# Optimization experiments

Hardware: AMD Instinct MI355X
Metric: run time of the kernel (lower is better)

Reference implementation:

```python
import jax, jax.numpy as jnp
import numpy as np

N_NODES = 100000
N_EDGES = 1250000
D_FEAT = 64

def setup_inputs() -> dict:
    key = jax.random.key(0)
    k1, k2, k3, k4 = jax.random.split(key, 4)
    src_x = jax.random.normal(k1, (N_NODES, D_FEAT), dtype=jnp.float32)
    dst_x = jax.random.normal(k2, (N_NODES, D_FEAT), dtype=jnp.float32)
    edge_index = jax.random.randint(k3, (2, N_EDGES), 0, N_NODES, dtype=jnp.int64)
    edge_weight = jax.random.uniform(k4, (N_EDGES, 1), dtype=jnp.float32)
    return {"src_x": src_x, "dst_x": dst_x, "edge_index": edge_index, "edge_weight": edge_weight}

def reference(src_x, dst_x, edge_index, edge_weight):
    # gather [E, d], scale by edge weight, scatter-add to destination nodes
    src_idx = edge_index[0]
    dst_idx = edge_index[1]
    msg = edge_weight * src_x[src_idx]            # [E, d]
    emb = jax.ops.segment_sum(msg, dst_idx, num_segments=dst_x.shape[0])  # [N_dst, d]
    return emb
```

## Files before the change

kernel.cpp:

```cpp
#include <hip/hip_runtime.h>

#define D_FEAT   64
#define BSHIFT   7
#define BROWS    (1 << BSHIFT)
#define SRC_MASK 0x1FFFFFF
#define CAPF     2816
#define CAPF_RAW 1920
#define OVF_CAP  16384
#define CAP_R5   2560
#define B_SC     512

__device__ __forceinline__ unsigned short f2bf(float f) {
    unsigned u = __float_as_uint(f);
    u += 0x7FFF + ((u >> 16) & 1);
    return (unsigned short)(u >> 16);
}
__device__ __forceinline__ float lo16f(unsigned u) { return __uint_as_float(u << 16); }
__device__ __forceinline__ float hi16f(unsigned u) { return __uint_as_float(u & 0xFFFF0000u); }
__device__ __forceinline__ float bf2f(unsigned short h) { return __uint_as_float(((unsigned)h) << 16); }

__global__ void lgconv_scatter_atomic(const float* __restrict__ src_x,
                                      const int* __restrict__ src_idx,
                                      const int* __restrict__ dst_idx,
                                      const float* __restrict__ ew,
                                      float* __restrict__ out,
                                      int n_edges) {
    int tid = blockIdx.x * blockDim.x + threadIdx.x;
    int edge = tid >> 4;
    int l    = tid & 15;
    if (edge >= n_edges) return;
    int s = src_idx[edge];
    int d = dst_idx[edge];
    float w = ew[edge];
    const float4 v = *reinterpret_cast<const float4*>(src_x + (size_t)s * D_FEAT + l * 4);
    float* o = out + (size_t)d * D_FEAT + l * 4;
    atomicAdd(o + 0, w * v.x);
    atomicAdd(o + 1, w * v.y);
    atomicAdd(o + 2, w * v.z);
    atomicAdd(o + 3, w * v.w);
}


__global__ void k_conv_hist(const float* __restrict__ src_x, unsigned short* __restrict__ sxb,
                            const int* __restrict__ dst, int* __restrict__ C,
                            int NE4, int E, int NB) {
    extern __shared__ int h[];
    int t = threadIdx.x, blk = blockIdx.x;
    int gsz = gridDim.x * blockDim.x;
    for (int i = blk * blockDim.x + t; i < NE4; i += gsz) {
        float4 v = reinterpret_cast<const float4*>(src_x)[i];
        ushort4 o;
        o.x = f2bf(v.x); o.y = f2bf(v.y); o.z = f2bf(v.z); o.w = f2bf(v.w);
        reinterpret_cast<ushort4*>(sxb)[i] = o;
    }
    for (int i = t; i < NB; i += blockDim.x) h[i] = 0;
    __syncthreads();
    int chunk = (E + gridDim.x - 1) / gridDim.x;
    int e0 = blk * chunk, e1 = min(E, e0 + chunk);
    for (int e = e0 + t; e < e1; e += blockDim.x)
        atomicAdd(&h[dst[e] >> BSHIFT], 1);
    __syncthreads();
    for (int i = t; i < NB; i += blockDim.x)
        C[i * B_SC + blk] = h[i];
}

__global__ void k_scan_det(int* __restrict__ C, int* __restrict__ btot,
                           int* __restrict__ ovf_cnt, int NB) {
    __shared__ int tmp[B_SC];
    int b = blockIdx.x, t = threadIdx.x;
    int v = C[b * B_SC + t];
    tmp[t] = v;
    __syncthreads();
    for (int d = 1; d < B_SC; d <<= 1) {
        int x = (t >= d) ? tmp[t - d] : 0;
        __syncthreads();
        tmp[t] += x;
        __syncthreads();
    }
    C[b * B_SC + t] = b * CAPF + tmp[t] - v;
    if (t == B_SC - 1) btot[b] = tmp[t];
    if (b == 0 && t == 0) *ovf_cnt = 0;
}

__global__ void k_scatter_det(const int* __restrict__ src, const int* __restrict__ dst,
                              const float* __restrict__ ew, const int* __restrict__ OFF,
                              int2* __restrict__ rec, int* __restrict__ ovf,
                              int* __restrict__ ovf_cnt, int E, int NB) {
    extern __shared__ int h[];
    int t = threadIdx.x, blk = blockIdx.x;
    for (int i = t; i < NB; i += blockDim.x) h[i] = OFF[i * B_SC + blk];
    __syncthreads();
    int chunk = (E + gridDim.x - 1) / gridDim.x;
    int e0 = blk * chunk, e1 = min(E, e0 + chunk);
    for (int e = e0 + t; e < e1; e += blockDim.x) {
        int d = dst[e];
        int b = d >> BSHIFT;
        int pos = atomicAdd(&h[b], 1);
        if (pos < b * CAPF + CAPF_RAW)
            rec[pos] = make_int2(src[e] | ((d & (BROWS - 1)) << 25),
                                 ((int)f2bf(ew[e])) << 16);
        else {
            int o = atomicAdd(ovf_cnt, 1);
            if (o < OVF_CAP) ovf[o] = e;
        }
    }
}

__global__ __launch_bounds__(512)
void k_sort_gather(const int* __restrict__ btot, const int2* __restrict__ rec,
                   const unsigned short* __restrict__ sxb,
                   const int* __restrict__ src, const int* __restrict__ dst,
                   const float* __restrict__ ew,
                   const int* __restrict__ ovf, const int* __restrict__ ovf_cnt,
                   float* __restrict__ out, int N) {
    __shared__ int2 S[CAPF_RAW];
    __shared__ int hist[BROWS];
    __shared__ int incl[BROWS];
    __shared__ int offl[BROWS];
    int b = blockIdx.x, t = threadIdx.x;
    int gbase = b * CAPF;
    int count = btot[b]; if (count > CAPF_RAW) count = CAPF_RAW;
    int nbase = b << BSHIFT;

    for (int i = t; i < BROWS; i += blockDim.x) hist[i] = 0;
    __syncthreads();
    for (int i = t; i < count; i += blockDim.x)
        atomicAdd(&hist[(rec[gbase + i].x >> 25) & (BROWS - 1)], 1);
    __syncthreads();
    if (t < BROWS) incl[t] = hist[t];
    __syncthreads();
    for (int d = 1; d < BROWS; d <<= 1) {
        int v = (t < BROWS && t >= d) ? incl[t - d] : 0;
        __syncthreads();
        if (t < BROWS) incl[t] += v;
        __syncthreads();
    }
    if (t < BROWS) {
        int ex = incl[t] - hist[t];
        offl[t] = ex;
        incl[t] = ex;
    }
    __syncthreads();
    for (int i = t; i < count; i += blockDim.x) {
        int2 r = rec[gbase + i];
        int pos = atomicAdd(&incl[(r.x >> 25) & (BROWS - 1)], 1);
        S[pos] = r;
    }
    __syncthreads();

    int wave = t >> 6, lane = t & 63;
    int grp = lane >> 3;
    int sub = lane & 7;

    for (int kb = wave * 16; kb < wave * 16 + 16; kb += 8) {
        int k    = kb + grp;
        int off  = offl[k];
        int deg  = hist[k];
        float a0 = 0.f, a1 = 0.f, a2 = 0.f, a3 = 0.f,
              a4 = 0.f, a5 = 0.f, a6 = 0.f, a7 = 0.f;

        for (int c = 0; __any(c < deg); c += 8) {
            int rs = 0; float rw = 0.f;
            if (c + sub < deg) {
                int2 r = S[off + c + sub];
                rs = r.x;
                rw = hi16f((unsigned)r.y);
            }
            #pragma unroll
            for (int i = 0; i < 8; ++i) {
                int jl = (grp << 3) + i;
                int   s = __shfl(rs, jl) & SRC_MASK;
                float w = __shfl(rw, jl);
                const uint4 u = *reinterpret_cast<const uint4*>(
                    sxb + (size_t)s * D_FEAT + sub * 8);
                a0 = fmaf(w, lo16f(u.x), a0); a1 = fmaf(w, hi16f(u.x), a1);
                a2 = fmaf(w, lo16f(u.y), a2); a3 = fmaf(w, hi16f(u.y), a3);
                a4 = fmaf(w, lo16f(u.z), a4); a5 = fmaf(w, hi16f(u.z), a5);
                a6 = fmaf(w, lo16f(u.w), a6); a7 = fmaf(w, hi16f(u.w), a7);
            }
        }
        int node = nbase + k;
        if (node < N) {
            float* o = out + (size_t)node * D_FEAT + sub * 8;
            *reinterpret_cast<float4*>(o)     = make_float4(a0, a1, a2, a3);
            *reinterpret_cast<float4*>(o + 4) = make_float4(a4, a5, a6, a7);
        }
    }

    __syncthreads();
    int n = *ovf_cnt; if (n > OVF_CAP) n = OVF_CAP;
    for (int idx = t; idx < n; idx += blockDim.x) {
        int e = ovf[idx];
        int d = dst[e];
        if ((d >> BSHIFT) != b) continue;
        float w = ew[e];
        int s = src[e];
        for (int q = 0; q < D_FEAT; ++q)
            atomicAdd(out + (size_t)d * D_FEAT + q,
                      w * bf2f(sxb[(size_t)s * D_FEAT + q]));
    }
}


__global__ void k_hist_b(const int* __restrict__ dst, int* __restrict__ counts_b,
                         int E, int NB) {
    extern __shared__ int h[];
    for (int i = threadIdx.x; i < NB; i += blockDim.x) h[i] = 0;
    __syncthreads();
    int chunk = (E + gridDim.x - 1) / gridDim.x;
    int e0 = blockIdx.x * chunk;
    int e1 = min(E, e0 + chunk);
    for (int e = e0 + threadIdx.x; e < e1; e += blockDim.x)
        atomicAdd(&h[dst[e] >> BSHIFT], 1);
    __syncthreads();
    for (int i = threadIdx.x; i < NB; i += blockDim.x)
        if (h[i]) atomicAdd(&counts_b[i], h[i]);
}

__global__ void k_scan_b(const int* __restrict__ counts, int* __restrict__ offsets,
                         int* __restrict__ cursor, int NB) {
    __shared__ int tmp[1024];
    __shared__ int carry;
    int t = threadIdx.x;
    if (t == 0) carry = 0;
    __syncthreads();
    for (int base = 0; base < NB; base += 1024) {
        int i = base + t;
        int v = (i < NB) ? counts[i] : 0;
        tmp[t] = v;
        __syncthreads();
        for (int d = 1; d < 1024; d <<= 1) {
            int x = (t >= d) ? tmp[t - d] : 0;
            __syncthreads();
            tmp[t] += x;
            __syncthreads();
        }
        int excl = tmp[t] - v + carry;
        if (i < NB) { offsets[i] = excl; cursor[i] = excl; }
        __syncthreads();
        if (t == 1023) carry += tmp[1023];
        __syncthreads();
    }
    if (t == 0) offsets[NB] = carry;
}

__global__ void k_scatter_b(const int* __restrict__ src, const int* __restrict__ dst,
                            const float* __restrict__ ew, int* __restrict__ cursor_b,
                            int2* __restrict__ rec, int E, int NB) {
    extern __shared__ int sh[];
    int* h    = sh;
    int* base = sh + NB;
    for (int i = threadIdx.x; i < NB; i += blockDim.x) h[i] = 0;
    __syncthreads();
    int chunk = (E + gridDim.x - 1) / gridDim.x;
    int e0 = blockIdx.x * chunk;
    int e1 = min(E, e0 + chunk);
    for (int e = e0 + threadIdx.x; e < e1; e += blockDim.x)
        atomicAdd(&h[dst[e] >> BSHIFT], 1);
    __syncthreads();
    for (int i = threadIdx.x; i < NB; i += blockDim.x) {
        int c = h[i];
        base[i] = c ? atomicAdd(&cursor_b[i], c) : 0;
        h[i] = 0;
    }
    __syncthreads();
    for (int e = e0 + threadIdx.x; e < e1; e += blockDim.x) {
        int d = dst[e];
        int b = d >> BSHIFT;
        int p = base[b] + atomicAdd(&h[b], 1);
        rec[p] = make_int2(src[e] | ((d & (BROWS - 1)) << 25), __float_as_int(ew[e]));
    }
}

__global__ void k_sort_bucket(const int* __restrict__ offsets_b, int2* __restrict__ rec,
                              int* __restrict__ node_off, int* __restrict__ node_cnt,
                              int N) {
    __shared__ int2 L[CAP_R5];
    __shared__ int hist[BROWS];
    __shared__ int incl[BROWS];
    int b = blockIdx.x, t = threadIdx.x;
    int base  = offsets_b[b];
    int end   = offsets_b[b + 1];
    int count = end - base;
    int nbase = b << BSHIFT;

    if (count > CAP_R5) {
        for (int i = t; i < BROWS; i += blockDim.x) {
            int n = nbase + i;
            if (n < N) { node_off[n] = -(base + 1); node_cnt[n] = count; }
        }
        return;
    }
    for (int i = t; i < BROWS; i += blockDim.x) hist[i] = 0;
    __syncthreads();
    for (int i = t; i < count; i += blockDim.x) {
        int2 r = rec[base + i];
        L[i] = r;
        atomicAdd(&hist[(r.x >> 25) & (BROWS - 1)], 1);
    }
    __syncthreads();
    if (t < BROWS) incl[t] = hist[t];
    __syncthreads();
    for (int d = 1; d < BROWS; d <<= 1) {
        int v = (t < BROWS && t >= d) ? incl[t - d] : 0;
        __syncthreads();
        if (t < BROWS) incl[t] += v;
        __syncthreads();
    }
    if (t < BROWS) {
        int ex = incl[t] - hist[t];
        int n  = nbase + t;
        if (n < N) { node_off[n] = base + ex; node_cnt[n] = hist[t]; }
        hist[t] = ex;
    }
    __syncthreads();
    for (int i = t; i < count; i += blockDim.x) {
        int2 r = L[i];
        int pos = atomicAdd(&hist[(r.x >> 25) & (BROWS - 1)], 1);
        rec[base + pos] = r;
    }
}

__global__ void k_gather(const float* __restrict__ src_x,
                         const int* __restrict__ node_off, const int* __restrict__ node_cnt,
                         const int2* __restrict__ rec,
                         float* __restrict__ out, int N) {
    int wid  = (blockIdx.x * blockDim.x + threadIdx.x) >> 6;
    int lane = threadIdx.x & 63;
    if (wid >= N) return;
    int off = node_off[wid];
    int deg = node_cnt[wid];
    float acc = 0.f;
    if (off >= 0) {
        for (int bseg = 0; bseg < deg; bseg += 64) {
            int m = deg - bseg;
            if (m > 64) m = 64;
            int2 r = (lane < m) ? rec[off + bseg + lane] : make_int2(0, 0);
            int   rs = r.x;
            float rw = __int_as_float(r.y);
            int i = 0;
            for (; i + 4 <= m; i += 4) {
                int s0 = __shfl(rs, i + 0) & SRC_MASK, s1 = __shfl(rs, i + 1) & SRC_MASK;
                int s2 = __shfl(rs, i + 2) & SRC_MASK, s3 = __shfl(rs, i + 3) & SRC_MASK;
                float w0 = __shfl(rw, i + 0), w1 = __shfl(rw, i + 1);
                float w2 = __shfl(rw, i + 2), w3 = __shfl(rw, i + 3);
                float v0 = src_x[(size_t)s0 * D_FEAT + lane];
                float v1 = src_x[(size_t)s1 * D_FEAT + lane];
                float v2 = src_x[(size_t)s2 * D_FEAT + lane];
                float v3 = src_x[(size_t)s3 * D_FEAT + lane];
                acc = fmaf(w0, v0, acc);
                acc = fmaf(w1, v1, acc);
                acc = fmaf(w2, v2, acc);
                acc = fmaf(w3, v3, acc);
            }
            for (; i < m; ++i) {
                int   s = __shfl(rs, i) & SRC_MASK;
                float w = __shfl(rw, i);
                acc = fmaf(w, src_x[(size_t)s * D_FEAT + lane], acc);
            }
        }
    } else {
        int base  = -off - 1;
        int local = wid & (BROWS - 1);
        for (int i = 0; i < deg; ++i) {
            int2 r = rec[base + i];
            if (((r.x >> 25) & (BROWS - 1)) == local)
                acc = fmaf(__int_as_float(r.y),
                           src_x[(size_t)(r.x & SRC_MASK) * D_FEAT + lane], acc);
        }
    }
    out[(size_t)wid * D_FEAT + lane] = acc;
}


extern "C" void kernel_launch(void* const* d_in, const int* in_sizes, int n_in,
                              void* d_out, int out_size, void* d_ws, size_t ws_size,
                              hipStream_t stream) {
    const float* src_x      = (const float*)d_in[0];
    const int*   edge_index = (const int*)d_in[2];
    const float* ew         = (const float*)d_in[3];
    float*       out        = (float*)d_out;

    const int E = in_sizes[3];
    const int N = in_sizes[1] / D_FEAT;
    const int* src = edge_index;
    const int* dst = edge_index + E;

    const int NB = (N + BROWS - 1) >> BSHIFT;
    auto align256 = [](size_t x) { return (x + 255) & ~(size_t)255; };
    const int block = 256;

    {
        size_t off = 0;
        size_t C_off      = off; off += align256((size_t)NB * B_SC * 4);
        size_t btot_off   = off; off += align256((size_t)NB * 4);
        size_t rec_off    = off; off += align256(((size_t)NB * CAPF + 64) * 8);
        size_t ovf_off    = off; off += align256((size_t)OVF_CAP * 4);
        size_t ovfc_off   = off; off += 256;
        size_t sxb_off    = off; off += align256((size_t)N * D_FEAT * 2);
        size_t need_full  = off;

        if (ws_size >= need_full && N <= (1 << 25) && (size_t)NB * 4 <= 60 * 1024) {
            char* w = (char*)d_ws;
            int*            C       = (int*)(w + C_off);
            int*            btot    = (int*)(w + btot_off);
            int2*           rec     = (int2*)(w + rec_off);
            int*            ovf     = (int*)(w + ovf_off);
            int*            ovf_cnt = (int*)(w + ovfc_off);
            unsigned short* sxb     = (unsigned short*)(w + sxb_off);

            const int NE4 = N * (D_FEAT / 4);
            k_conv_hist<<<B_SC, block, (size_t)NB * 4, stream>>>(src_x, sxb, dst, C, NE4, E, NB);
            k_scan_det<<<NB, B_SC, 0, stream>>>(C, btot, ovf_cnt, NB);
            k_scatter_det<<<B_SC, block, (size_t)NB * 4, stream>>>(src, dst, ew, C, rec,
                                                                   ovf, ovf_cnt, E, NB);
            k_sort_gather<<<NB, 512, 0, stream>>>(btot, rec, sxb, src, dst, ew,
                                                  ovf, ovf_cnt, out, N);
            return;
        }
    }

    {
        size_t off = 0;
        size_t counts_off  = off; off += align256((size_t)NB * 4);
        size_t offsets_off = off; off += align256((size_t)(NB + 1) * 4);
        size_t cursor_off  = off; off += align256((size_t)NB * 4);
        size_t noff_off    = off; off += align256((size_t)N * 4);
        size_t ncnt_off    = off; off += align256((size_t)N * 4);
        size_t rec_off     = off; off += align256((size_t)E * 8);
        size_t need_r5 = off;

        if (ws_size >= need_r5 && N <= (1 << 25) && (size_t)NB * 8 <= 60 * 1024) {
            char* w = (char*)d_ws;
            int*  counts_b  = (int*)(w + counts_off);
            int*  offsets_b = (int*)(w + offsets_off);
            int*  cursor_b  = (int*)(w + cursor_off);
            int*  node_off  = (int*)(w + noff_off);
            int*  node_cnt  = (int*)(w + ncnt_off);
            int2* rec       = (int2*)(w + rec_off);

            hipMemsetAsync(counts_b, 0, (size_t)NB * 4, stream);
            const int B = 256;
            k_hist_b<<<B, block, (size_t)NB * 4, stream>>>(dst, counts_b, E, NB);
            k_scan_b<<<1, 1024, 0, stream>>>(counts_b, offsets_b, cursor_b, NB);
            k_scatter_b<<<B, block, (size_t)NB * 8, stream>>>(src, dst, ew, cursor_b, rec, E, NB);
            k_sort_bucket<<<NB, block, 0, stream>>>(offsets_b, rec, node_off, node_cnt, N);
            k_gather<<<(N + 3) / 4, 256, 0, stream>>>(src_x, node_off, node_cnt, rec, out, N);
            return;
        }
    }

    hipMemsetAsync(d_out, 0, (size_t)out_size * sizeof(float), stream);
    const long long total = (long long)E * 16;
    const int grid = (int)((total + block - 1) / block);
    lgconv_scatter_atomic<<<grid, block, 0, stream>>>(src_x, src, dst, ew, out, E);
}
```

Before: 70.67 us.

## Split each 128-row bucket across two blocks handling 64 destination rows each

The sort-gather kernel now launches two blocks per destination bucket, each filtering the bucket's records to its own 64-row half, sorting them into a smaller shared buffer and accumulating one row per 8-lane group. This doubles the number of blocks and halves shared memory per block, aiming for more parallelism and better occupancy in the gather phase. In exchange, each bucket's records are read twice from global memory. A slow per-row linear scan fallback is added for when a half overflows the shared buffer.

```diff
diff --git a/kernel.cpp b/kernel.cpp
--- a/kernel.cpp
+++ b/kernel.cpp
@@ -6,6 +6,7 @@
 #define SRC_MASK 0x1FFFFFF
 #define CAPF     2816
 #define CAPF_RAW 1920
+#define SCAP     1280
 #define OVF_CAP  16384
 #define CAP_R5   2560
 #define B_SC     512
@@ -113,52 +114,62 @@
                    const float* __restrict__ ew,
                    const int* __restrict__ ovf, const int* __restrict__ ovf_cnt,
                    float* __restrict__ out, int N) {
-    __shared__ int2 S[CAPF_RAW];
-    __shared__ int hist[BROWS];
-    __shared__ int incl[BROWS];
-    __shared__ int offl[BROWS];
-    int b = blockIdx.x, t = threadIdx.x;
+    __shared__ int2 S[SCAP];
+    __shared__ int hist[64];
+    __shared__ int incl[64];
+    __shared__ int offl[64];
+    int bb = blockIdx.x;
+    int b = bb >> 1, half = bb & 1;
+    int t = threadIdx.x;
     int gbase = b * CAPF;
     int count = btot[b]; if (count > CAPF_RAW) count = CAPF_RAW;
-    int nbase = b << BSHIFT;
-
-    for (int i = t; i < BROWS; i += blockDim.x) hist[i] = 0;
-    __syncthreads();
-    for (int i = t; i < count; i += blockDim.x)
-        atomicAdd(&hist[(rec[gbase + i].x >> 25) & (BROWS - 1)], 1);
-    __syncthreads();
-    if (t < BROWS) incl[t] = hist[t];
-    __syncthreads();
-    for (int d = 1; d < BROWS; d <<= 1) {
-        int v = (t < BROWS && t >= d) ? incl[t - d] : 0;
-        __syncthreads();
-        if (t < BROWS) incl[t] += v;
-        __syncthreads();
-    }
-    if (t < BROWS) {
+    int nbase = (b << BSHIFT) + half * 64;
+
+    if (t < 64) hist[t] = 0;
+    __syncthreads();
+    for (int i = t; i < count; i += 512) {
+        int node = (rec[gbase + i].x >> 25) & (BROWS - 1);
+        if ((node >> 6) == half) atomicAdd(&hist[node & 63], 1);
+    }
+    __syncthreads();
+    if (t < 64) incl[t] = hist[t];
+    __syncthreads();
+    for (int d = 1; d < 64; d <<= 1) {
+        int v = (t < 64 && t >= d) ? incl[t - d] : 0;
+        __syncthreads();
+        if (t < 64) incl[t] += v;
+        __syncthreads();
+    }
+    if (t < 64) {
         int ex = incl[t] - hist[t];
         offl[t] = ex;
         incl[t] = ex;
     }
     __syncthreads();
-    for (int i = t; i < count; i += blockDim.x) {
-        int2 r = rec[gbase + i];
-        int pos = atomicAdd(&incl[(r.x >> 25) & (BROWS - 1)], 1);
-        S[pos] = r;
+    int half_total = offl[63] + hist[63];
+    bool fits = (half_total <= SCAP);
+    if (fits) {
+        for (int i = t; i < count; i += 512) {
+            int2 r = rec[gbase + i];
+            int node = (r.x >> 25) & (BROWS - 1);
+            if ((node >> 6) == half) {
+                int pos = atomicAdd(&incl[node & 63], 1);
+                S[pos] = r;
+            }
+        }
     }
     __syncthreads();
 
     int wave = t >> 6, lane = t & 63;
     int grp = lane >> 3;
     int sub = lane & 7;
-
-    for (int kb = wave * 16; kb < wave * 16 + 16; kb += 8) {
-        int k    = kb + grp;
-        int off  = offl[k];
-        int deg  = hist[k];
-        float a0 = 0.f, a1 = 0.f, a2 = 0.f, a3 = 0.f,
-              a4 = 0.f, a5 = 0.f, a6 = 0.f, a7 = 0.f;
-
+    int k   = wave * 8 + grp;
+    int off = offl[k];
+    int deg = hist[k];
+    float a0 = 0.f, a1 = 0.f, a2 = 0.f, a3 = 0.f,
+          a4 = 0.f, a5 = 0.f, a6 = 0.f, a7 = 0.f;
+
+    if (fits) {
         for (int c = 0; __any(c < deg); c += 8) {
             int rs = 0; float rw = 0.f;
             if (c + sub < deg) {
@@ -179,20 +190,36 @@
                 a6 = fmaf(w, lo16f(u.w), a6); a7 = fmaf(w, hi16f(u.w), a7);
             }
         }
-        int node = nbase + k;
-        if (node < N) {
-            float* o = out + (size_t)node * D_FEAT + sub * 8;
-            *reinterpret_cast<float4*>(o)     = make_float4(a0, a1, a2, a3);
-            *reinterpret_cast<float4*>(o + 4) = make_float4(a4, a5, a6, a7);
-        }
+    } else {
+        int want = half * 64 + k;
+        for (int i = 0; i < count; ++i) {
+            int2 r = rec[gbase + i];
+            if (((r.x >> 25) & (BROWS - 1)) == want) {
+                float w = hi16f((unsigned)r.y);
+                int   s = r.x & SRC_MASK;
+                const uint4 u = *reinterpret_cast<const uint4*>(
+                    sxb + (size_t)s * D_FEAT + sub * 8);
+                a0 = fmaf(w, lo16f(u.x), a0); a1 = fmaf(w, hi16f(u.x), a1);
+                a2 = fmaf(w, lo16f(u.y), a2); a3 = fmaf(w, hi16f(u.y), a3);
+                a4 = fmaf(w, lo16f(u.z), a4); a5 = fmaf(w, hi16f(u.z), a5);
+                a6 = fmaf(w, lo16f(u.w), a6); a7 = fmaf(w, hi16f(u.w), a7);
+            }
+        }
+    }
+    int node = nbase + k;
+    if (node < N) {
+        float* o = out + (size_t)node * D_FEAT + sub * 8;
+        *reinterpret_cast<float4*>(o)     = make_float4(a0, a1, a2, a3);
+        *reinterpret_cast<float4*>(o + 4) = make_float4(a4, a5, a6, a7);
     }
 
     __syncthreads();
     int n = *ovf_cnt; if (n > OVF_CAP) n = OVF_CAP;
-    for (int idx = t; idx < n; idx += blockDim.x) {
+    for (int idx = t; idx < n; idx += 512) {
         int e = ovf[idx];
         int d = dst[e];
         if ((d >> BSHIFT) != b) continue;
+        if (((d & (BROWS - 1)) >> 6) != half) continue;
         float w = ew[e];
         int s = src[e];
         for (int q = 0; q < D_FEAT; ++q)
@@ -414,8 +441,8 @@
             k_scan_det<<<NB, B_SC, 0, stream>>>(C, btot, ovf_cnt, NB);
             k_scatter_det<<<B_SC, block, (size_t)NB * 4, stream>>>(src, dst, ew, C, rec,
                                                                    ovf, ovf_cnt, E, NB);
-            k_sort_gather<<<NB, 512, 0, stream>>>(btot, rec, sxb, src, dst, ew,
-                                                  ovf, ovf_cnt, out, N);
+            k_sort_gather<<<2 * NB, 512, 0, stream>>>(btot, rec, sxb, src, dst, ew,
+                                                      ovf, ovf_cnt, out, N);
             return;
         }
     }
```

Result: slower. 77.08 us (+9.1%).
